# Kernel optimization log

Hardware: AMD Instinct MI355X
Metric: run time of the kernel (lower is better)

The kernel has to match this reference:

```python
import jax, jax.numpy as jnp
import numpy as np

N, D = 4096, 1024

def setup_inputs() -> dict:
    key = jax.random.key(0)
    k0, k1, k2, k3 = jax.random.split(key, 4)
    s = 1.0 / np.sqrt(D)
    return {
        "x": jax.random.normal(k0, (N, D), dtype=jnp.float32),
        "Wq": jax.random.normal(k1, (D, N), dtype=jnp.float32) * s,
        "Wk": jax.random.normal(k2, (D, N), dtype=jnp.float32) * s,
        "Wv": jax.random.normal(k3, (D, N), dtype=jnp.float32) * s,
    }

def reference(x, Wq, Wk, Wv):
    # Projections: (N, D) @ (D, N) -> (N, N)
    q = x @ Wq
    k = x @ Wk
    v = x @ Wv
    # score[i, j] = q_i . k_j  -> softmax over axis=1 (per query row)
    score = q @ k.T                      # (N, N)
    p = jax.nn.softmax(score, axis=1)    # (N, N)
    # Original: sum_i v[i, :] * softmax(score)^T[i, j]  == p @ v  (N, N)
    # (the broadcast outer-product+sum is mathematically a matmul)
    return p @ v
```

## Files before the change

kernel.cpp:

```cpp
#include <hip/hip_runtime.h>
#include <hip/hip_bf16.h>
#include <stdint.h>

typedef __attribute__((ext_vector_type(8))) short short8v;
typedef __attribute__((ext_vector_type(8))) _Float16 half8v;
typedef __attribute__((ext_vector_type(4))) float f32x4;

__device__ __forceinline__ unsigned short f2bf(float f) {
  unsigned u = __builtin_bit_cast(unsigned, f);
  unsigned r = 0x7fffu + ((u >> 16) & 1u);
  return (unsigned short)((u + r) >> 16);
}
__device__ __forceinline__ float bf2f(unsigned short h) {
  unsigned u = ((unsigned)h) << 16;
  return __builtin_bit_cast(float, u);
}
__device__ __forceinline__ unsigned short f2h(float f) {
  _Float16 h = (_Float16)f;
  return __builtin_bit_cast(unsigned short, h);
}
__device__ __forceinline__ void gload_lds16(const void* g, void* l) {
  __builtin_amdgcn_global_load_lds(
      (const __attribute__((address_space(1))) void*)g,
      (__attribute__((address_space(3))) void*)l, 16, 0, 0);
}
#define SBAR  __builtin_amdgcn_s_barrier()
#define SCHED __builtin_amdgcn_sched_barrier(0)

__global__ __launch_bounds__(256) void split_plain(
    const float4* __restrict__ X, ushort4* __restrict__ H, ushort4* __restrict__ L, int n4) {
  int idx = blockIdx.x * 256 + threadIdx.x;
  if (idx >= n4) return;
  float4 v = X[idx];
  ushort4 h, l;
  h.x = f2bf(v.x); l.x = f2bf(v.x - bf2f(h.x));
  h.y = f2bf(v.y); l.y = f2bf(v.y - bf2f(h.y));
  h.z = f2bf(v.z); l.z = f2bf(v.z - bf2f(h.z));
  h.w = f2bf(v.w); l.w = f2bf(v.w - bf2f(h.w));
  H[idx] = h; L[idx] = l;
}

__global__ __launch_bounds__(256) void split_x3(
    const float4* __restrict__ X, ushort4* __restrict__ H, ushort4* __restrict__ L,
    ushort4* __restrict__ F, int n4) {
  int idx = blockIdx.x * 256 + threadIdx.x;
  if (idx >= n4) return;
  float4 v = X[idx];
  ushort4 h, l, f;
  h.x = f2bf(v.x); l.x = f2bf(v.x - bf2f(h.x)); f.x = f2h(v.x);
  h.y = f2bf(v.y); l.y = f2bf(v.y - bf2f(h.y)); f.y = f2h(v.y);
  h.z = f2bf(v.z); l.z = f2bf(v.z - bf2f(h.z)); f.z = f2h(v.z);
  h.w = f2bf(v.w); l.w = f2bf(v.w - bf2f(h.w)); f.w = f2h(v.w);
  H[idx] = h; L[idx] = l; F[idx] = f;
}

template<bool WL>
__global__ __launch_bounds__(256) void split_T(
    const float* __restrict__ W, unsigned short* __restrict__ H,
    unsigned short* __restrict__ L, int Kd, int Nd) {
  __shared__ float tile[32][33];
  const int t = threadIdx.x;
  const int c = t & 31;
  const int r0 = t >> 5;
  const int k0 = blockIdx.y * 32, n0 = blockIdx.x * 32;
#pragma unroll
  for (int i = 0; i < 4; ++i) {
    int r = r0 + i * 8;
    tile[r][c] = W[(size_t)(k0 + r) * Nd + n0 + c];
  }
  __syncthreads();
#pragma unroll
  for (int i = 0; i < 4; ++i) {
    int n = r0 + i * 8;
    float f = tile[c][n];
    unsigned short h = f2bf(f);
    size_t o = (size_t)(n0 + n) * Kd + k0 + c;
    H[o] = h;
    if (WL) L[o] = f2bf(f - bf2f(h));
  }
}

__global__ __launch_bounds__(256) void reduceT_M(
    const float* __restrict__ P, unsigned short* __restrict__ H,
    unsigned short* __restrict__ L, int nsplit) {
  __shared__ float tile[32][33];
  const int t = threadIdx.x;
  const int c = t & 31;
  const int r0 = t >> 5;
  const int a0 = blockIdx.y * 32, b0 = blockIdx.x * 32;
#pragma unroll
  for (int i = 0; i < 4; ++i) {
    int r = r0 + i * 8;
    float s = 0.f;
    for (int sp = 0; sp < nsplit; ++sp)
      s += P[(size_t)sp * 1048576 + (size_t)(a0 + r) * 1024 + b0 + c];
    tile[r][c] = s;
  }
  __syncthreads();
#pragma unroll
  for (int i = 0; i < 4; ++i) {
    int b = r0 + i * 8;
    float f = tile[c][b];
    unsigned short h = f2bf(f);
    size_t o = (size_t)(b0 + b) * 1024 + a0 + c;
    H[o] = h;
    L[o] = f2bf(f - bf2f(h));
  }
}

__global__ __launch_bounds__(256) void reduce_f16(
    const float4* __restrict__ P, ushort4* __restrict__ H,
    int n4, int nsplit, int stride4) {
  int idx = blockIdx.x * 256 + threadIdx.x;
  if (idx >= n4) return;
  float4 s = P[idx];
  for (int sp = 1; sp < nsplit; ++sp) {
    float4 v = P[(size_t)sp * stride4 + idx];
    s.x += v.x; s.y += v.y; s.z += v.z; s.w += v.w;
  }
  ushort4 h;
  h.x = f2h(s.x); h.y = f2h(s.y); h.z = f2h(s.z); h.w = f2h(s.w);
  H[idx] = h;
}

__global__ __launch_bounds__(256) void reduce_bf16(
    const float4* __restrict__ P, ushort4* __restrict__ H,
    int n4, int nsplit, int stride4) {
  int idx = blockIdx.x * 256 + threadIdx.x;
  if (idx >= n4) return;
  float4 s = P[idx];
  for (int sp = 1; sp < nsplit; ++sp) {
    float4 v = P[(size_t)sp * stride4 + idx];
    s.x += v.x; s.y += v.y; s.z += v.z; s.w += v.w;
  }
  ushort4 h;
  h.x = f2bf(s.x); h.y = f2bf(s.y); h.z = f2bf(s.z); h.w = f2bf(s.w);
  H[idx] = h;
}

template<bool SWZ>
__global__ __launch_bounds__(512, 1) void gemm_fused3(
    const unsigned short* __restrict__ base,
    unsigned dAh, unsigned dAl, unsigned dBh, unsigned dBl,
    int N, int K, int kchunk, int tilesX,
    float* __restrict__ Cf, size_t partStride) {
  __shared__ unsigned short lds[65536];
  const int AH = 0, BH = 8192, BL = 16384, AL = 24576;
  const int NT = kchunk >> 5;
  const int wg = blockIdx.x;
  int bx, by;
  if (SWZ) { const int sw = ((wg & 7) << 5) | (wg >> 3); bx = sw & 15; by = sw >> 4; }
  else     { bx = wg % tilesX; by = wg / tilesX; }
  const int m0 = by << 8, n0 = bx << 8;
  const unsigned koff = (unsigned)blockIdx.y * (unsigned)kchunk;
  Cf += (size_t)blockIdx.y * partStride;

  const int tid = threadIdx.x;
  const int w = tid >> 6, lane = tid & 63;
  const int wr = w >> 2, wc = w & 3;
  const int lr = lane & 15;
  const int phys = (lane >> 4) ^ ((lr >> 1) & 3);
  const int aoff = (wr * 128 + lr) * 32 + phys * 8;
  const int boff = (wc * 64 + lr) * 32 + phys * 8;
  const int rst = tid >> 2;
  const int ssrc = ((tid & 3) ^ ((tid >> 3) & 3)) * 8;
  const unsigned jstep = 128u * (unsigned)K;

  const unsigned voffA = (unsigned)(m0 + rst) * (unsigned)K + (unsigned)ssrc + koff;
  const unsigned voffB = (unsigned)(n0 + rst) * (unsigned)K + (unsigned)ssrc + koff;

  f32x4 acc[8][4];
#pragma unroll
  for (int m = 0; m < 8; ++m)
#pragma unroll
    for (int n = 0; n < 4; ++n) acc[m][n] = {0.f, 0.f, 0.f, 0.f};

#define STG2(dsel, vo, loff, s, tt) do {                                     \
    const unsigned o_ = (vo) + (dsel) + (unsigned)(tt) * 32u;                \
    gload_lds16(base + o_,         &lds[(s) + (loff) + (w << 9)]);           \
    gload_lds16(base + o_ + jstep, &lds[(s) + (loff) + 4096 + (w << 9)]);    \
  } while (0)

  STG2(dAh, voffA, AH, 0, 0);
  STG2(dBl, voffB, BL, 0, 0);
  STG2(dBh, voffB, BH, 0, 0);
  STG2(dAl, voffA, AL, 0, 0);

  for (int t = 0; t < NT; ++t) {
    const int slot = (t & 1) << 15;
    const int slot1 = ((t + 1) & 1) << 15;
    const bool st = (t + 1) < NT;
    short8v ahf[8];
    SCHED; asm volatile("s_waitcnt vmcnt(4)"); SBAR; SCHED;
    {
      short8v bf[4];
#pragma unroll
      for (int n = 0; n < 4; ++n)
        bf[n] = *(const short8v*)&lds[slot + BL + boff + n * 512];
#pragma unroll
      for (int m = 0; m < 8; ++m)
        ahf[m] = *(const short8v*)&lds[slot + AH + aoff + m * 512];
      if (st) { STG2(dAh, voffA, AH, slot1, t + 1); STG2(dBl, voffB, BL, slot1, t + 1); }
      __builtin_amdgcn_s_setprio(1);
#pragma unroll
      for (int m = 0; m < 8; ++m)
#pragma unroll
        for (int n = 0; n < 4; ++n)
          acc[m][n] = __builtin_amdgcn_mfma_f32_16x16x32_bf16(ahf[m], bf[n], acc[m][n], 0, 0, 0);
      __builtin_amdgcn_s_setprio(0);
    }
    SCHED;
    if (st) { asm volatile("s_waitcnt vmcnt(6)"); }
    else    { asm volatile("s_waitcnt vmcnt(2)"); }
    SBAR; SCHED;
    short8v bh[4];
    {
#pragma unroll
      for (int n = 0; n < 4; ++n)
        bh[n] = *(const short8v*)&lds[slot + BH + boff + n * 512];
      if (st) { STG2(dBh, voffB, BH, slot1, t + 1); }
      __builtin_amdgcn_s_setprio(1);
#pragma unroll
      for (int m = 0; m < 8; ++m)
#pragma unroll
        for (int n = 0; n < 4; ++n)
          acc[m][n] = __builtin_amdgcn_mfma_f32_16x16x32_bf16(ahf[m], bh[n], acc[m][n], 0, 0, 0);
      __builtin_amdgcn_s_setprio(0);
    }
    SCHED;
    if (st) { asm volatile("s_waitcnt vmcnt(6)"); }
    else    { asm volatile("s_waitcnt vmcnt(0)"); }
    SBAR; SCHED;
    {
      short8v alf[8];
#pragma unroll
      for (int m = 0; m < 8; ++m)
        alf[m] = *(const short8v*)&lds[slot + AL + aoff + m * 512];
      if (st) { STG2(dAl, voffA, AL, slot1, t + 1); }
      __builtin_amdgcn_s_setprio(1);
#pragma unroll
      for (int m = 0; m < 8; ++m)
#pragma unroll
        for (int n = 0; n < 4; ++n)
          acc[m][n] = __builtin_amdgcn_mfma_f32_16x16x32_bf16(alf[m], bh[n], acc[m][n], 0, 0, 0);
      __builtin_amdgcn_s_setprio(0);
    }
    SCHED;
  }
#undef STG2

  const int crow = m0 + wr * 128 + ((lane >> 4) << 2);
  const int ccol = n0 + wc * 64 + lr;
#pragma unroll
  for (int mi = 0; mi < 8; ++mi)
#pragma unroll
    for (int r = 0; r < 4; ++r) {
      const int row = crow + mi * 16 + r;
#pragma unroll
      for (int n = 0; n < 4; ++n)
        Cf[(size_t)row * N + ccol + n * 16] = acc[mi][n][r];
    }
}

template<bool SWZ, int DT>
__global__ __launch_bounds__(256, 2) void gemm_plain128(
    const unsigned short* __restrict__ A, const unsigned short* __restrict__ B,
    int N, int K, int kchunk, int tilesX,
    float* __restrict__ Cf, size_t partStride) {
  __shared__ unsigned short lds[32768];
  const int NT = kchunk >> 5;
  const int wg = blockIdx.x;
  int bx, by;
  if (SWZ) { const int sw = ((wg & 7) << 7) | (wg >> 3); bx = sw & 31; by = sw >> 5; }
  else     { bx = wg % tilesX; by = wg / tilesX; }
  const int m0 = by << 7, n0 = bx << 7;
  const unsigned koff = (unsigned)blockIdx.y * (unsigned)kchunk;
  Cf += (size_t)blockIdx.y * partStride;

  const int tid = threadIdx.x;
  const int w = tid >> 6, lane = tid & 63;
  const int wr = w >> 1, wc = w & 1;
  const int lr = lane & 15;
  const int phys = (lane >> 4) ^ ((lr >> 1) & 3);
  const int aoff = (wr * 64 + lr) * 32 + phys * 8;
  const int boff = 4096 + (wc * 64 + lr) * 32 + phys * 8;
  const int rst = w * 16 + (lane >> 2);
  const int ssrc = ((lane & 3) ^ ((lane >> 3) & 3)) * 8;

  f32x4 acc[4][4];
#pragma unroll
  for (int m = 0; m < 4; ++m)
#pragma unroll
    for (int n = 0; n < 4; ++n) acc[m][n] = {0.f, 0.f, 0.f, 0.f};

  const unsigned short* gA = A + (size_t)(m0 + rst) * K + ssrc + koff;
  const unsigned short* gB = B + (size_t)(n0 + rst) * K + ssrc + koff;
  const size_t jstep = (size_t)64 * K;

#define MFMA_DT(af, bf, c) (DT == 1 ? \
    __builtin_amdgcn_mfma_f32_16x16x32_f16(__builtin_bit_cast(half8v, af), \
        __builtin_bit_cast(half8v, bf), (c), 0, 0, 0) : \
    __builtin_amdgcn_mfma_f32_16x16x32_bf16((af), (bf), (c), 0, 0, 0))

#pragma unroll
  for (int tau = 0; tau < 3; ++tau) {
    const int so = tau * 8192 + (w << 9);
    gload_lds16(gA + (size_t)tau * 32, &lds[so]);
    gload_lds16(gA + (size_t)tau * 32 + jstep, &lds[so + 2048]);
    gload_lds16(gB + (size_t)tau * 32, &lds[so + 4096]);
    gload_lds16(gB + (size_t)tau * 32 + jstep, &lds[so + 6144]);
  }
  asm volatile("s_waitcnt vmcnt(8)");
  SCHED; SBAR; SCHED;

  for (int t = 0; t < NT; ++t) {
    const int sb = (t & 3) * 8192;
    if (t + 3 < NT) {
      const int so = ((t + 3) & 3) * 8192 + (w << 9);
      const unsigned short* srcA = gA + (size_t)(t + 3) * 32;
      const unsigned short* srcB = gB + (size_t)(t + 3) * 32;
      gload_lds16(srcA, &lds[so]);
      gload_lds16(srcA + jstep, &lds[so + 2048]);
      gload_lds16(srcB, &lds[so + 4096]);
      gload_lds16(srcB + jstep, &lds[so + 6144]);
    }
    short8v bfr[4], af[4];
#pragma unroll
    for (int n = 0; n < 4; ++n)
      bfr[n] = *(const short8v*)&lds[sb + boff + n * 512];
#pragma unroll
    for (int m = 0; m < 4; ++m)
      af[m] = *(const short8v*)&lds[sb + aoff + m * 512];
    __builtin_amdgcn_s_setprio(1);
#pragma unroll
    for (int m = 0; m < 4; ++m)
#pragma unroll
      for (int n = 0; n < 4; ++n)
        acc[m][n] = MFMA_DT(af[m], bfr[n], acc[m][n]);
    __builtin_amdgcn_s_setprio(0);
    SCHED;
    if (t < NT - 3)       { asm volatile("s_waitcnt vmcnt(8)"); }
    else if (t == NT - 3) { asm volatile("s_waitcnt vmcnt(4)"); }
    else if (t == NT - 2) { asm volatile("s_waitcnt vmcnt(0)"); }
    SCHED;
    if (t < NT - 1) { SBAR; SCHED; }
  }
#undef MFMA_DT

  const int crow = m0 + wr * 64 + ((lane >> 4) << 2);
  const int ccol = n0 + wc * 64 + lr;
#pragma unroll
  for (int mi = 0; mi < 4; ++mi)
#pragma unroll
    for (int r = 0; r < 4; ++r) {
      const int row = crow + mi * 16 + r;
#pragma unroll
      for (int n = 0; n < 4; ++n)
        Cf[(size_t)row * N + ccol + n * 16] = acc[mi][n][r];
    }
}

__global__ __launch_bounds__(256) void softmax_rows(
    const float* __restrict__ S, unsigned short* __restrict__ P, int n) {
  const int row = blockIdx.x;
  const int t = threadIdx.x;
  const float4* src = (const float4*)(S + (size_t)row * n);
  float4 v[4];
  float mx = -3.0e38f;
#pragma unroll
  for (int i = 0; i < 4; ++i) {
    v[i] = src[i * 256 + t];
    mx = fmaxf(mx, fmaxf(fmaxf(v[i].x, v[i].y), fmaxf(v[i].z, v[i].w)));
  }
#pragma unroll
  for (int off = 32; off; off >>= 1) mx = fmaxf(mx, __shfl_xor(mx, off));
  __shared__ float redm[4], reds[4];
  const int wid = t >> 6, lane = t & 63;
  if (lane == 0) redm[wid] = mx;
  __syncthreads();
  mx = fmaxf(fmaxf(redm[0], redm[1]), fmaxf(redm[2], redm[3]));
  float sum = 0.f;
#pragma unroll
  for (int i = 0; i < 4; ++i) {
    v[i].x = __expf(v[i].x - mx);
    v[i].y = __expf(v[i].y - mx);
    v[i].z = __expf(v[i].z - mx);
    v[i].w = __expf(v[i].w - mx);
    sum += (v[i].x + v[i].y) + (v[i].z + v[i].w);
  }
#pragma unroll
  for (int off = 32; off; off >>= 1) sum += __shfl_xor(sum, off);
  if (lane == 0) reds[wid] = sum;
  __syncthreads();
  sum = (reds[0] + reds[1]) + (reds[2] + reds[3]);
  float inv = 1.0f / sum;
#pragma unroll
  for (int i = 0; i < 4; ++i) {
    ushort4 o;
    o.x = f2bf(v[i].x * inv);
    o.y = f2bf(v[i].y * inv);
    o.z = f2bf(v[i].z * inv);
    o.w = f2bf(v[i].w * inv);
    *(ushort4*)(P + (size_t)row * n + (size_t)(i * 256 + t) * 4) = o;
  }
}

extern "C" void kernel_launch(void* const* d_in, const int* in_sizes, int n_in,
                              void* d_out, int out_size, void* d_ws, size_t ws_size,
                              hipStream_t stream) {
  (void)in_sizes; (void)n_in; (void)out_size; (void)ws_size;
  const float* x  = (const float*)d_in[0];
  const float* Wq = (const float*)d_in[1];
  const float* Wk = (const float*)d_in[2];
  const float* Wv = (const float*)d_in[3];
  const int N = 4096, D = 1024;
  const size_t MB = 1ull << 20;
  const unsigned MEL = (unsigned)(MB / 2);
  char* ws = (char*)d_ws;
  unsigned short* xh  = (unsigned short*)(ws + 0 * MB);
  unsigned short* xl  = (unsigned short*)(ws + 8 * MB);
  unsigned short* wqh = (unsigned short*)(ws + 16 * MB);
  unsigned short* wql = (unsigned short*)(ws + 24 * MB);
  unsigned short* wkh = (unsigned short*)(ws + 32 * MB);
  unsigned short* wkl = (unsigned short*)(ws + 40 * MB);
  unsigned short* wvh = (unsigned short*)(ws + 48 * MB);
  unsigned short* Mth = (unsigned short*)(ws + 56 * MB);
  unsigned short* Mtl = (unsigned short*)(ws + 58 * MB);
  unsigned short* p   = (unsigned short*)(ws + 64 * MB);
  float*          Mpart = (float*)(ws + 96 * MB);
  float*          ypart = (float*)(ws + 96 * MB);
  float*          zpart = (float*)(ws + 96 * MB);
  unsigned short* y16 = (unsigned short*)(ws + 16 * MB);
  unsigned short* zh  = (unsigned short*)(ws + 32 * MB);
  unsigned short* xTh = (unsigned short*)(ws + 160 * MB);
  unsigned short* x16 = (unsigned short*)(ws + 184 * MB);
  float* score = (float*)d_out;
  float* out   = (float*)d_out;

  split_x3<<<4096, 256, 0, stream>>>((const float4*)x, (ushort4*)xh, (ushort4*)xl,
                                     (ushort4*)x16, 1048576);
  split_plain<<<4096, 256, 0, stream>>>((const float4*)Wq, (ushort4*)wqh, (ushort4*)wql, 1048576);
  split_plain<<<4096, 256, 0, stream>>>((const float4*)Wk, (ushort4*)wkh, (ushort4*)wkl, 1048576);
  split_T<false><<<dim3(N / 32, D / 32), 256, 0, stream>>>(Wv, wvh, nullptr, D, N);
  split_T<false><<<dim3(D / 32, N / 32), 256, 0, stream>>>(x, xTh, nullptr, N, D);

  gemm_fused3<false><<<dim3(16, 16), 512, 0, stream>>>(
      wqh, 0u, 8 * MEL, 16 * MEL, 24 * MEL,
      1024, 4096, 256, 4, Mpart, (size_t)1024 * 1024);
  reduceT_M<<<dim3(32, 32), 256, 0, stream>>>(Mpart, Mth, Mtl, 16);

  gemm_fused3<false><<<dim3(64, 4), 512, 0, stream>>>(
      xh, 0u, 8 * MEL, 56 * MEL, 58 * MEL,
      1024, 1024, 256, 4, ypart, (size_t)4096 * 1024);
  reduce_f16<<<4096, 256, 0, stream>>>(
      (const float4*)ypart, (ushort4*)y16, 1048576, 4, 1048576);

  gemm_plain128<true, 1><<<dim3(1024, 1), 256, 0, stream>>>(
      y16, x16, N, 1024, 1024, 32, score, 0);

  softmax_rows<<<N, 256, 0, stream>>>(score, p, N);

  gemm_plain128<false, 0><<<dim3(256, 4), 256, 0, stream>>>(
      p, xTh, 1024, 4096, 1024, 8, zpart, (size_t)4096 * 1024);
  reduce_bf16<<<4096, 256, 0, stream>>>(
      (const float4*)zpart, (ushort4*)zh, 1048576, 4, 1048576);

  gemm_plain128<true, 0><<<dim3(1024, 1), 256, 0, stream>>>(
      zh, wvh, N, 1024, 1024, 32, out, 0);
}
```

Measured before the change: 316.7 us.

## Enlarge plain GEMM tiles to 256x256 with 8 waves and XCD-aware swizzle

Converts the 128x128, 4-wave GEMM into a 256x256, 8-wave kernel where each wave computes a 128x64 sub-tile (8x4 MFMA accumulators), doubling LDS staging to 128 KB. It also replaces the tile swizzle with one that groups 2x2 tile blocks per XCD. The aim is higher arithmetic intensity per LDS/global load and better L2 locality across XCDs. In exchange it launches only 256 workgroups on a 256-CU part, raises register and LDS pressure, and limits occupancy to one block per CU.

```diff
diff --git a/kernel.cpp b/kernel.cpp
--- a/kernel.cpp
+++ b/kernel.cpp
@@ -263,39 +263,43 @@
 }
 
 template<bool SWZ, int DT>
-__global__ __launch_bounds__(256, 2) void gemm_plain128(
+__global__ __launch_bounds__(512, 2) void gemm_plain(
     const unsigned short* __restrict__ A, const unsigned short* __restrict__ B,
     int N, int K, int kchunk, int tilesX,
     float* __restrict__ Cf, size_t partStride) {
-  __shared__ unsigned short lds[32768];
+  __shared__ unsigned short lds[65536];
   const int NT = kchunk >> 5;
   const int wg = blockIdx.x;
   int bx, by;
-  if (SWZ) { const int sw = ((wg & 7) << 7) | (wg >> 3); bx = sw & 31; by = sw >> 5; }
-  else     { bx = wg % tilesX; by = wg / tilesX; }
-  const int m0 = by << 7, n0 = bx << 7;
+  if (SWZ) {
+    const int xcd = wg & 7, idx = wg >> 3;
+    const int sg = (idx >> 2) * 8 + xcd;
+    by = ((sg >> 3) << 1) + ((idx >> 1) & 1);
+    bx = ((sg & 7) << 1) + (idx & 1);
+  } else { bx = wg % tilesX; by = wg / tilesX; }
+  const int m0 = by << 8, n0 = bx << 8;
   const unsigned koff = (unsigned)blockIdx.y * (unsigned)kchunk;
   Cf += (size_t)blockIdx.y * partStride;
 
   const int tid = threadIdx.x;
   const int w = tid >> 6, lane = tid & 63;
-  const int wr = w >> 1, wc = w & 1;
+  const int wr = w >> 2, wc = w & 3;
   const int lr = lane & 15;
   const int phys = (lane >> 4) ^ ((lr >> 1) & 3);
-  const int aoff = (wr * 64 + lr) * 32 + phys * 8;
-  const int boff = 4096 + (wc * 64 + lr) * 32 + phys * 8;
+  const int aoff = (wr * 128 + lr) * 32 + phys * 8;
+  const int boff = 8192 + (wc * 64 + lr) * 32 + phys * 8;
   const int rst = w * 16 + (lane >> 2);
   const int ssrc = ((lane & 3) ^ ((lane >> 3) & 3)) * 8;
 
-  f32x4 acc[4][4];
-#pragma unroll
-  for (int m = 0; m < 4; ++m)
+  f32x4 acc[8][4];
+#pragma unroll
+  for (int m = 0; m < 8; ++m)
 #pragma unroll
     for (int n = 0; n < 4; ++n) acc[m][n] = {0.f, 0.f, 0.f, 0.f};
 
   const unsigned short* gA = A + (size_t)(m0 + rst) * K + ssrc + koff;
   const unsigned short* gB = B + (size_t)(n0 + rst) * K + ssrc + koff;
-  const size_t jstep = (size_t)64 * K;
+  const size_t jstep = (size_t)128 * K;
 
 #define MFMA_DT(af, bf, c) (DT == 1 ? \
     __builtin_amdgcn_mfma_f32_16x16x32_f16(__builtin_bit_cast(half8v, af), \
@@ -304,39 +308,47 @@
 
 #pragma unroll
   for (int tau = 0; tau < 3; ++tau) {
-    const int so = tau * 8192 + (w << 9);
+    const int so = tau * 16384 + (w << 9);
     gload_lds16(gA + (size_t)tau * 32, &lds[so]);
-    gload_lds16(gA + (size_t)tau * 32 + jstep, &lds[so + 2048]);
-    gload_lds16(gB + (size_t)tau * 32, &lds[so + 4096]);
-    gload_lds16(gB + (size_t)tau * 32 + jstep, &lds[so + 6144]);
+    gload_lds16(gA + (size_t)tau * 32 + jstep, &lds[so + 4096]);
+    gload_lds16(gB + (size_t)tau * 32, &lds[so + 8192]);
+    gload_lds16(gB + (size_t)tau * 32 + jstep, &lds[so + 12288]);
   }
   asm volatile("s_waitcnt vmcnt(8)");
   SCHED; SBAR; SCHED;
 
   for (int t = 0; t < NT; ++t) {
-    const int sb = (t & 3) * 8192;
+    const int sb = (t & 3) * 16384;
     if (t + 3 < NT) {
-      const int so = ((t + 3) & 3) * 8192 + (w << 9);
+      const int so = ((t + 3) & 3) * 16384 + (w << 9);
       const unsigned short* srcA = gA + (size_t)(t + 3) * 32;
       const unsigned short* srcB = gB + (size_t)(t + 3) * 32;
       gload_lds16(srcA, &lds[so]);
-      gload_lds16(srcA + jstep, &lds[so + 2048]);
-      gload_lds16(srcB, &lds[so + 4096]);
-      gload_lds16(srcB + jstep, &lds[so + 6144]);
-    }
-    short8v bfr[4], af[4];
+      gload_lds16(srcA + jstep, &lds[so + 4096]);
+      gload_lds16(srcB, &lds[so + 8192]);
+      gload_lds16(srcB + jstep, &lds[so + 12288]);
+    }
+    short8v bfr[4], af0[4], af1[4];
 #pragma unroll
     for (int n = 0; n < 4; ++n)
       bfr[n] = *(const short8v*)&lds[sb + boff + n * 512];
 #pragma unroll
     for (int m = 0; m < 4; ++m)
-      af[m] = *(const short8v*)&lds[sb + aoff + m * 512];
+      af0[m] = *(const short8v*)&lds[sb + aoff + m * 512];
+#pragma unroll
+    for (int m = 0; m < 4; ++m)
+      af1[m] = *(const short8v*)&lds[sb + aoff + 2048 + m * 512];
     __builtin_amdgcn_s_setprio(1);
 #pragma unroll
     for (int m = 0; m < 4; ++m)
 #pragma unroll
       for (int n = 0; n < 4; ++n)
-        acc[m][n] = MFMA_DT(af[m], bfr[n], acc[m][n]);
+        acc[m][n] = MFMA_DT(af0[m], bfr[n], acc[m][n]);
+#pragma unroll
+    for (int m = 0; m < 4; ++m)
+#pragma unroll
+      for (int n = 0; n < 4; ++n)
+        acc[4 + m][n] = MFMA_DT(af1[m], bfr[n], acc[4 + m][n]);
     __builtin_amdgcn_s_setprio(0);
     SCHED;
     if (t < NT - 3)       { asm volatile("s_waitcnt vmcnt(8)"); }
@@ -347,10 +359,10 @@
   }
 #undef MFMA_DT
 
-  const int crow = m0 + wr * 64 + ((lane >> 4) << 2);
+  const int crow = m0 + wr * 128 + ((lane >> 4) << 2);
   const int ccol = n0 + wc * 64 + lr;
 #pragma unroll
-  for (int mi = 0; mi < 4; ++mi)
+  for (int mi = 0; mi < 8; ++mi)
 #pragma unroll
     for (int r = 0; r < 4; ++r) {
       const int row = crow + mi * 16 + r;
@@ -455,16 +467,16 @@
   reduce_f16<<<4096, 256, 0, stream>>>(
       (const float4*)ypart, (ushort4*)y16, 1048576, 4, 1048576);
 
-  gemm_plain128<true, 1><<<dim3(1024, 1), 256, 0, stream>>>(
-      y16, x16, N, 1024, 1024, 32, score, 0);
+  gemm_plain<true, 1><<<dim3(256, 1), 512, 0, stream>>>(
+      y16, x16, N, 1024, 1024, 16, score, 0);
 
   softmax_rows<<<N, 256, 0, stream>>>(score, p, N);
 
-  gemm_plain128<false, 0><<<dim3(256, 4), 256, 0, stream>>>(
-      p, xTh, 1024, 4096, 1024, 8, zpart, (size_t)4096 * 1024);
+  gemm_plain<false, 0><<<dim3(64, 4), 512, 0, stream>>>(
+      p, xTh, 1024, 4096, 1024, 4, zpart, (size_t)4096 * 1024);
   reduce_bf16<<<4096, 256, 0, stream>>>(
       (const float4*)zpart, (ushort4*)zh, 1048576, 4, 1048576);
 
-  gemm_plain128<true, 0><<<dim3(1024, 1), 256, 0, stream>>>(
-      zh, wvh, N, 1024, 1024, 32, out, 0);
-}
+  gemm_plain<true, 0><<<dim3(256, 1), 512, 0, stream>>>(
+      zh, wvh, N, 1024, 1024, 16, out, 0);
+}
```

Result: faster. 292.0 us (-7.8%).
